# Kernel tuning notes

Measured on AMD Instinct MI355X. Metric: run time of the kernel, lower is better.

Reference implementation:

```python
import jax, jax.numpy as jnp
import numpy as np

N_NODES = 110
C = 4096  # in_channels = hidden = out_channels


def setup_inputs() -> dict:
    key = jax.random.key(0)
    ks = jax.random.split(key, 8)
    x = jax.random.normal(ks[0], (N_NODES, C), dtype=jnp.float32)
    adj = jax.random.randint(ks[1], (N_NODES, N_NODES), 0, 2, dtype=jnp.int32)
    # torch.nn.Linear weights stored [out_features, in_features]
    W2 = jax.random.normal(ks[2], (C, C), dtype=jnp.float32) / np.sqrt(C)
    b2 = jax.random.normal(ks[3], (C,), dtype=jnp.float32) * 0.01
    W1 = jax.random.normal(ks[4], (2 * C, C), dtype=jnp.float32) / np.sqrt(2 * C)
    b1 = jax.random.normal(ks[5], (C,), dtype=jnp.float32) * 0.01
    Wl = jax.random.normal(ks[6], (N_NODES, N_NODES), dtype=jnp.float32) / np.sqrt(N_NODES)
    bl = jax.random.normal(ks[7], (N_NODES,), dtype=jnp.float32) * 0.01
    # note: W1 is stored [in=2C, out=C]; W2 [in=C, out=C]; Wl [in=110, out=110]
    return {"x": x, "adj": adj, "W2": W2, "b2": b2, "W1": W1, "b1": b1, "Wl": Wl, "bl": bl}


def reference(x, adj, W2, b2, W1, b1, Wl, bl):
    # FeatGraphConv: h = lin2(x)
    h = x @ W2 + b2  # [N, C]
    # edge_index.nonzero(): adjacency -> edge list (i=src, j=dst); mean-aggregate
    # h[src] at dst. Dense equivalent: column-normalized mask matmul.
    mask = (adj != 0).astype(x.dtype)  # [N, N]
    deg = mask.sum(axis=0)  # in-degree of each target node j
    aggr = (mask.T @ h) / jnp.maximum(deg, 1.0)[:, None]  # [N, C]; 0 for isolated nodes (PyG mean)
    # update: lin1(cat(h, aggr)) then relu (in RegGNN.forward)
    out = jax.nn.relu(jnp.concatenate([h, aggr], axis=1) @ W1 + b1)  # [N, C]
    # x.t(); lin(110,110); x.t()
    out = (out.T @ Wl.T + bl).T  # [N, C]
    return out
```

## Files before the change

### kernel.cpp

```cpp
#include <hip/hip_runtime.h>
#include <hip/hip_fp16.h>

#define C 4096
#define NN 110
#define MPAD 112
#define BN 128
#define BK 64
#define KCHUNK 512
#define LDSTR 72

typedef _Float16 f16x8 __attribute__((ext_vector_type(8)));
typedef float fx4 __attribute__((ext_vector_type(4)));

__global__ void prep1_kernel(const float* __restrict__ x, _Float16* __restrict__ A1) {
    int idx = blockIdx.x * 256 + threadIdx.x;
    int n = idx >> 12;
    float v = (n < NN) ? x[idx] : 0.f;
    A1[idx] = (_Float16)v;
}

__global__ __launch_bounds__(256, 2)
void mm_kernel(const _Float16* __restrict__ A, const float* __restrict__ B,
               float* __restrict__ Cacc, int lda) {
    __shared__ _Float16 As[MPAD * LDSTR];
    __shared__ _Float16 Bs[BN * LDSTR];

    const int t  = threadIdx.x;
    const int j0 = blockIdx.x * BN;
    const int k0 = blockIdx.y * KCHUNK;
    const int w   = t >> 6;
    const int L   = t & 63;
    const int l15 = L & 15;
    const int q   = L >> 4;

    const int bc  = t & 127;
    const int bgq = t >> 7;

    fx4 acc[7][2];
    #pragma unroll
    for (int mt = 0; mt < 7; ++mt)
        #pragma unroll
        for (int nt = 0; nt < 2; ++nt)
            acc[mt][nt] = (fx4){0.f, 0.f, 0.f, 0.f};

    for (int kc = 0; kc < KCHUNK; kc += BK) {
        {
            int idx = t;
            #pragma unroll
            for (int i = 0; i < 4; ++i) {
                if (idx < MPAD * (BK / 8)) {
                    int row = idx >> 3;
                    int ko  = (idx & 7) << 3;
                    *(f16x8*)(As + row * LDSTR + ko) =
                        *(const f16x8*)(A + (size_t)row * lda + k0 + kc + ko);
                }
                idx += 256;
            }
        }
        {
            #pragma unroll
            for (int p = 0; p < 16; ++p) {
                int r = (bgq * 16 + p) * 2;
                float v0 = B[(size_t)(k0 + kc + r) * C + j0 + bc];
                float v1 = B[(size_t)(k0 + kc + r + 1) * C + j0 + bc];
                union { _Float16 h[2]; unsigned u; } pk;
                pk.h[0] = (_Float16)v0;
                pk.h[1] = (_Float16)v1;
                *(unsigned*)(Bs + bc * LDSTR + r) = pk.u;
            }
        }
        __syncthreads();
        #pragma unroll
        for (int s = 0; s < 2; ++s) {
            const int ko = s * 32 + q * 8;
            f16x8 bfrag[2];
            #pragma unroll
            for (int nt = 0; nt < 2; ++nt)
                bfrag[nt] = *(const f16x8*)(Bs + (w * 32 + nt * 16 + l15) * LDSTR + ko);
            #pragma unroll
            for (int mt = 0; mt < 7; ++mt) {
                f16x8 afrag = *(const f16x8*)(As + (mt * 16 + l15) * LDSTR + ko);
                #pragma unroll
                for (int nt = 0; nt < 2; ++nt)
                    acc[mt][nt] = __builtin_amdgcn_mfma_f32_16x16x32_f16(
                        afrag, bfrag[nt], acc[mt][nt], 0, 0, 0);
            }
        }
        __syncthreads();
    }

    #pragma unroll
    for (int mt = 0; mt < 7; ++mt) {
        #pragma unroll
        for (int nt = 0; nt < 2; ++nt) {
            const int col = j0 + w * 32 + nt * 16 + l15;
            #pragma unroll
            for (int r = 0; r < 4; ++r) {
                int row = mt * 16 + q * 4 + r;
                if (row < NN)
                    atomicAdd(&Cacc[(size_t)row * C + col], acc[mt][nt][r]);
            }
        }
    }
}

__global__ __launch_bounds__(256)
void agg_kernel(const float* __restrict__ h_raw, const int* __restrict__ adj,
                const float* __restrict__ b2, _Float16* __restrict__ A3) {
    __shared__ float hb[NN * 16];
    __shared__ unsigned long long mlo[NN], mhi[NN];
    __shared__ float degs[NN];
    const int t  = threadIdx.x;
    const int c0 = blockIdx.x * 16;

    for (int idx = t; idx < NN * 16; idx += 256) {
        int n = idx >> 4, c = idx & 15;
        float v = h_raw[(size_t)n * C + c0 + c] + b2[c0 + c];
        hb[idx] = v;
        A3[(size_t)n * (2 * C) + c0 + c] = (_Float16)v;
    }
    if (t < 64) {
        int n  = NN + (t >> 5);
        int hs = (t >> 4) & 1;
        int c  = t & 15;
        A3[(size_t)n * (2 * C) + hs * C + c0 + c] = (_Float16)0.f;
    }
    if (t < NN) {
        int j = t;
        unsigned long long lo = 0, hi = 0;
        int dg = 0;
        for (int i = 0; i < 64; ++i) {
            int m = (adj[i * NN + j] != 0);
            lo |= ((unsigned long long)m) << i; dg += m;
        }
        for (int i = 64; i < NN; ++i) {
            int m = (adj[i * NN + j] != 0);
            hi |= ((unsigned long long)m) << (i - 64); dg += m;
        }
        mlo[j] = lo; mhi[j] = hi;
        degs[j] = (float)(dg > 0 ? dg : 1);
    }
    __syncthreads();
    for (int idx = t; idx < NN * 16; idx += 256) {
        int j = idx >> 4, c = idx & 15;
        unsigned long long lo = mlo[j], hi = mhi[j];
        float a = 0.f;
        for (int i = 0; i < 64; ++i)
            if ((lo >> i) & 1) a += hb[i * 16 + c];
        for (int i = 64; i < NN; ++i)
            if ((hi >> (i - 64)) & 1) a += hb[i * 16 + c];
        A3[(size_t)j * (2 * C) + C + c0 + c] = (_Float16)(a / degs[j]);
    }
}

__global__ __launch_bounds__(256)
void fin_kernel(const float* __restrict__ z_raw, const float* __restrict__ b1,
                const float* __restrict__ Wl, const float* __restrict__ bl,
                float* __restrict__ out) {
    __shared__ float zs[NN * 64];
    const int t  = threadIdx.x;
    const int c0 = blockIdx.x * 64;
    const int j  = blockIdx.y * 4 + (t >> 6);
    const int c  = t & 63;

    for (int idx = t; idx < NN * 64; idx += 256) {
        int k = idx >> 6, cc = idx & 63;
        float v = z_raw[(size_t)k * C + c0 + cc] + b1[c0 + cc];
        zs[idx] = fmaxf(v, 0.f);
    }
    __syncthreads();
    if (j < NN) {
        float a = bl[j];
        #pragma unroll 2
        for (int k = 0; k < NN; ++k)
            a += Wl[j * NN + k] * zs[k * 64 + c];
        out[(size_t)j * C + c0 + c] = a;
    }
}

extern "C" void kernel_launch(void* const* d_in, const int* in_sizes, int n_in,
                              void* d_out, int out_size, void* d_ws, size_t ws_size,
                              hipStream_t stream) {
    const float* x   = (const float*)d_in[0];
    const int*   adj = (const int*)d_in[1];
    const float* W2  = (const float*)d_in[2];
    const float* b2  = (const float*)d_in[3];
    const float* W1  = (const float*)d_in[4];
    const float* b1  = (const float*)d_in[5];
    const float* Wl  = (const float*)d_in[6];
    const float* bl  = (const float*)d_in[7];
    float* out = (float*)d_out;

    char* ws = (char*)d_ws;
    float*    h_raw = (float*)(ws);
    float*    z_raw = (float*)(ws + 1802240);
    _Float16* A1    = (_Float16*)(ws + 3604480);
    _Float16* A3    = (_Float16*)(ws + 4521984);

    hipMemsetAsync(d_ws, 0, 3604480, stream);
    prep1_kernel<<<(MPAD * C) / 256, 256, 0, stream>>>(x, A1);
    mm_kernel<<<dim3(C / BN, C / KCHUNK), 256, 0, stream>>>(A1, W2, h_raw, C);
    agg_kernel<<<C / 16, 256, 0, stream>>>(h_raw, adj, b2, A3);
    mm_kernel<<<dim3(C / BN, (2 * C) / KCHUNK), 256, 0, stream>>>(A3, W1, z_raw, 2 * C);
    fin_kernel<<<dim3(C / 64, 28), 256, 0, stream>>>(z_raw, b1, Wl, bl, out);
}
```

Before: 379.1 us.

## Replace LDS-tiled GEMM with per-wave register-pipelined split-K GEMM

The skinny GEMM kernel no longer stages A and B tiles through shared memory with block-wide barriers. Each wave now owns a 16-column strip and a K chunk, loads A fragments and B values straight from global memory into registers, and double-buffers them so the next loads overlap the current MFMAs. The intent is to remove LDS traffic and __syncthreads stalls in this memory-bound GEMM with only 110 rows. In exchange, each wave re-reads the A matrix from global/L2, B loads are strided per lane, and the split-K factor and grid shape change, which affects the number of atomic adds.

```diff
diff --git a/kernel.cpp b/kernel.cpp
--- a/kernel.cpp
+++ b/kernel.cpp
@@ -4,10 +4,6 @@
 #define C 4096
 #define NN 110
 #define MPAD 112
-#define BN 128
-#define BK 64
-#define KCHUNK 512
-#define LDSTR 72
 
 typedef _Float16 f16x8 __attribute__((ext_vector_type(8)));
 typedef float fx4 __attribute__((ext_vector_type(4)));
@@ -21,85 +17,63 @@
 
 __global__ __launch_bounds__(256, 2)
 void mm_kernel(const _Float16* __restrict__ A, const float* __restrict__ B,
-               float* __restrict__ Cacc, int lda) {
-    __shared__ _Float16 As[MPAD * LDSTR];
-    __shared__ _Float16 Bs[BN * LDSTR];
-
-    const int t  = threadIdx.x;
-    const int j0 = blockIdx.x * BN;
-    const int k0 = blockIdx.y * KCHUNK;
-    const int w   = t >> 6;
+               float* __restrict__ Cacc, int lda, int kch) {
+    const int t   = threadIdx.x;
+    const int wid = blockIdx.x * 4 + (t >> 6);
     const int L   = t & 63;
     const int l15 = L & 15;
     const int q   = L >> 4;
+    const int n0  = (wid & 255) * 16;
+    const int k0  = (wid >> 8) * kch;
 
-    const int bc  = t & 127;
-    const int bgq = t >> 7;
+    const _Float16* Ap = A + (size_t)l15 * lda + k0 + q * 8;
+    const float*    Bp = B + (size_t)(k0 + q * 8) * C + n0 + l15;
 
-    fx4 acc[7][2];
+    fx4 acc[7];
     #pragma unroll
-    for (int mt = 0; mt < 7; ++mt)
+    for (int mt = 0; mt < 7; ++mt) acc[mt] = (fx4){0.f, 0.f, 0.f, 0.f};
+
+    float bv0[8], bv1[8];
+    f16x8 av0[7], av1[7];
+
+    auto loadB = [&](float (&bv)[8], int kk) {
         #pragma unroll
-        for (int nt = 0; nt < 2; ++nt)
-            acc[mt][nt] = (fx4){0.f, 0.f, 0.f, 0.f};
+        for (int j = 0; j < 8; ++j) bv[j] = Bp[(size_t)(kk + j) * C];
+    };
+    auto loadA = [&](f16x8 (&av)[7], int kk) {
+        #pragma unroll
+        for (int mt = 0; mt < 7; ++mt)
+            av[mt] = *(const f16x8*)(Ap + (size_t)(mt * 16) * lda + kk);
+    };
+    auto consume = [&](float (&bv)[8], f16x8 (&av)[7]) {
+        f16x8 bf;
+        #pragma unroll
+        for (int j = 0; j < 8; ++j) bf[j] = (_Float16)bv[j];
+        #pragma unroll
+        for (int mt = 0; mt < 7; ++mt)
+            acc[mt] = __builtin_amdgcn_mfma_f32_16x16x32_f16(av[mt], bf, acc[mt], 0, 0, 0);
+    };
 
-    for (int kc = 0; kc < KCHUNK; kc += BK) {
-        {
-            int idx = t;
-            #pragma unroll
-            for (int i = 0; i < 4; ++i) {
-                if (idx < MPAD * (BK / 8)) {
-                    int row = idx >> 3;
-                    int ko  = (idx & 7) << 3;
-                    *(f16x8*)(As + row * LDSTR + ko) =
-                        *(const f16x8*)(A + (size_t)row * lda + k0 + kc + ko);
-                }
-                idx += 256;
-            }
+    loadB(bv0, 0);
+    loadA(av0, 0);
+    for (int k = 0; k < kch; k += 64) {
+        loadB(bv1, k + 32);
+        loadA(av1, k + 32);
+        consume(bv0, av0);
+        if (k + 64 < kch) {
+            loadB(bv0, k + 64);
+            loadA(av0, k + 64);
         }
-        {
-            #pragma unroll
-            for (int p = 0; p < 16; ++p) {
-                int r = (bgq * 16 + p) * 2;
-                float v0 = B[(size_t)(k0 + kc + r) * C + j0 + bc];
-                float v1 = B[(size_t)(k0 + kc + r + 1) * C + j0 + bc];
-                union { _Float16 h[2]; unsigned u; } pk;
-                pk.h[0] = (_Float16)v0;
-                pk.h[1] = (_Float16)v1;
-                *(unsigned*)(Bs + bc * LDSTR + r) = pk.u;
-            }
-        }
-        __syncthreads();
-        #pragma unroll
-        for (int s = 0; s < 2; ++s) {
-            const int ko = s * 32 + q * 8;
-            f16x8 bfrag[2];
-            #pragma unroll
-            for (int nt = 0; nt < 2; ++nt)
-                bfrag[nt] = *(const f16x8*)(Bs + (w * 32 + nt * 16 + l15) * LDSTR + ko);
-            #pragma unroll
-            for (int mt = 0; mt < 7; ++mt) {
-                f16x8 afrag = *(const f16x8*)(As + (mt * 16 + l15) * LDSTR + ko);
-                #pragma unroll
-                for (int nt = 0; nt < 2; ++nt)
-                    acc[mt][nt] = __builtin_amdgcn_mfma_f32_16x16x32_f16(
-                        afrag, bfrag[nt], acc[mt][nt], 0, 0, 0);
-            }
-        }
-        __syncthreads();
+        consume(bv1, av1);
     }
 
     #pragma unroll
     for (int mt = 0; mt < 7; ++mt) {
         #pragma unroll
-        for (int nt = 0; nt < 2; ++nt) {
-            const int col = j0 + w * 32 + nt * 16 + l15;
-            #pragma unroll
-            for (int r = 0; r < 4; ++r) {
-                int row = mt * 16 + q * 4 + r;
-                if (row < NN)
-                    atomicAdd(&Cacc[(size_t)row * C + col], acc[mt][nt][r]);
-            }
+        for (int r = 0; r < 4; ++r) {
+            int row = mt * 16 + q * 4 + r;
+            if (row < NN)
+                atomicAdd(&Cacc[(size_t)row * C + n0 + l15], acc[mt][r]);
         }
     }
 }
@@ -199,8 +173,8 @@
 
     hipMemsetAsync(d_ws, 0, 3604480, stream);
     prep1_kernel<<<(MPAD * C) / 256, 256, 0, stream>>>(x, A1);
-    mm_kernel<<<dim3(C / BN, C / KCHUNK), 256, 0, stream>>>(A1, W2, h_raw, C);
+    mm_kernel<<<512, 256, 0, stream>>>(A1, W2, h_raw, C, 512);
     agg_kernel<<<C / 16, 256, 0, stream>>>(h_raw, adj, b2, A3);
-    mm_kernel<<<dim3(C / BN, (2 * C) / KCHUNK), 256, 0, stream>>>(A3, W1, z_raw, 2 * C);
+    mm_kernel<<<512, 256, 0, stream>>>(A3, W1, z_raw, 2 * C, 1024);
     fin_kernel<<<dim3(C / 64, 28), 256, 0, stream>>>(z_raw, b1, Wl, bl, out);
 }
```

Measured after the change: 391.3 us. 3.2% more time.
